# Performance work log

Hardware: AMD Instinct MI355X
Metric: run time of the kernel (lower is better)

Reference implementation:

```python
import jax, jax.numpy as jnp
import numpy as np

N_NODES = 50000
N_EDGES = 150000
HID = 512

def _gelu(x):
    return jax.nn.gelu(x, approximate=False)  # torch nn.GELU default is exact erf

def setup_inputs() -> dict:
    key = jax.random.key(0)
    ks = jax.random.split(key, 12)
    s = 0.02
    return {
        "node_features": jax.random.normal(ks[0], (N_NODES, HID), jnp.float32),
        "river_features": jax.random.normal(ks[1], (N_NODES, 3), jnp.float32),
        "river_edges": jax.random.randint(ks[2], (N_EDGES, 2), 0, N_NODES, jnp.int64),
        "W1": jax.random.normal(ks[3], (HID + 3, HID), jnp.float32) * s,
        "b1": jnp.zeros((HID,), jnp.float32),
        "W2": jax.random.normal(ks[4], (HID, HID), jnp.float32) * s,
        "b2": jnp.zeros((HID,), jnp.float32),
        "Wm1": jax.random.normal(ks[5], (2 * HID, HID), jnp.float32) * s,
        "bm1": jnp.zeros((HID,), jnp.float32),
        "Wm2": jax.random.normal(ks[6], (HID, HID), jnp.float32) * s,
        "bm2": jnp.zeros((HID,), jnp.float32),
    }

def _message_pass(features, edges, Wm1, bm1, Wm2, bm2):
    src = features[edges[:, 0]]   # [E, H] gather
    tgt = features[edges[:, 1]]   # [E, H] gather
    h = _gelu(jnp.concatenate([src, tgt], axis=-1) @ Wm1 + bm1)
    messages = h @ Wm2 + bm2      # [E, H]
    # the original per-edge python loop `new_features[tgt] += messages[i]` is a scatter-add
    return features + jax.ops.segment_sum(messages, edges[:, 1], num_segments=features.shape[0])

def reference(node_features, river_features, river_edges, W1, b1, W2, b2, Wm1, bm1, Wm2, bm2):
    x = jnp.concatenate([node_features, river_features], axis=-1)  # [N, H+3]
    feats = _gelu(x @ W1 + b1) @ W2 + b2                           # river_encoder
    for _ in range(3):
        feats = _message_pass(feats, river_edges, Wm1, bm1, Wm2, bm2)
    return feats
```

## Files before the change

### kernel.cpp

```cpp
#include <hip/hip_runtime.h>
#include <hip/hip_bf16.h>
#include <cstdint>

using u16 = unsigned short;
typedef short s16x8 __attribute__((ext_vector_type(8)));
typedef float f32x4 __attribute__((ext_vector_type(4)));

__device__ __forceinline__ float b2f(u16 b) {
    union { unsigned u; float f; } z; z.u = ((unsigned)b) << 16; return z.f;
}
__device__ __forceinline__ u16 f2b(float f) {
    union { float f; unsigned u; } z; z.f = f;
    return (u16)((z.u + 0x7fffu + ((z.u >> 16) & 1u)) >> 16);
}
__device__ __forceinline__ float gelu_f(float x) {
    return 0.5f * x * (1.0f + erff(x * 0.70710678118654752440f));
}
__device__ __forceinline__ void gl2lds16(const void* g, void* l) {
    __builtin_amdgcn_global_load_lds(
        (const __attribute__((address_space(1))) void*)g,
        (__attribute__((address_space(3))) void*)l, 16, 0, 0);
}

enum { F_BIAS = 1, F_GELU = 2, F_RANK3 = 4, F_RESIDH = 8,
       F_DEG = 16, F_OUTF = 32, F_OUTH = 64 };

template<int EPI>
__global__ __launch_bounds__(256, 4) void gemm_k(
    const u16* __restrict__ A, const u16* __restrict__ Bt,
    float* __restrict__ Cf, u16* __restrict__ Ch,
    const u16* __restrict__ srcH,
    const float* __restrict__ bias, const float* __restrict__ bias2,
    const int* __restrict__ deg, const float* __restrict__ river,
    const float* __restrict__ w1tail, int Mreal, int ldh, int gxShift)
{
    __shared__ __align__(16) u16 As[128 * 32];
    __shared__ __align__(16) u16 Bs[128 * 32];

    const int nwg  = gridDim.x;
    const int orig = blockIdx.x;
    const int xcd  = orig & 7;
    const int i    = orig >> 3;
    const int q    = nwg >> 3;
    const int r    = nwg & 7;
    const int swz  = (xcd < r) ? (xcd * (q + 1) + i) : (r * (q + 1) + (xcd - r) * q + i);
    const int rowblk = swz >> gxShift;
    const int colblk = swz & ((1 << gxShift) - 1);

    const int tid  = threadIdx.x;
    const int lane = tid & 63;
    const int wid  = tid >> 6;
    const int wr   = wid >> 1;
    const int wc   = wid & 1;
    const int fr   = lane & 15;
    const int fq   = lane >> 4;

    const long arow = (long)rowblk * 128 + (wid << 4) + (lane >> 2);
    const long brow = (long)colblk * 128 + (wid << 4) + (lane >> 2);
    const int  kofs = (lane & 3) << 3;
    u16* asw = As + (wid << 9);
    u16* bsw = Bs + (wid << 9);

    f32x4 acc[4][4];
#pragma unroll
    for (int m = 0; m < 4; m++)
#pragma unroll
        for (int n = 0; n < 4; n++) { f32x4 z = {0.f, 0.f, 0.f, 0.f}; acc[m][n] = z; }

    for (int kt = 0; kt < 512; kt += 32) {
        gl2lds16(A  + arow * 512 + kt + kofs,        asw);
        gl2lds16(A  + (arow + 64) * 512 + kt + kofs, asw + 2048);
        gl2lds16(Bt + brow * 512 + kt + kofs,        bsw);
        gl2lds16(Bt + (brow + 64) * 512 + kt + kofs, bsw + 2048);
        __syncthreads();

        s16x8 af[4], bf[4];
#pragma unroll
        for (int m = 0; m < 4; m++)
            af[m] = *(const s16x8*)(As + (((wr << 6) + (m << 4) + fr) << 5) + (fq << 3));
#pragma unroll
        for (int n = 0; n < 4; n++)
            bf[n] = *(const s16x8*)(Bs + (((wc << 6) + (n << 4) + fr) << 5) + (fq << 3));
#pragma unroll
        for (int m = 0; m < 4; m++)
#pragma unroll
            for (int n = 0; n < 4; n++)
                acc[m][n] = __builtin_amdgcn_mfma_f32_16x16x32_bf16(af[m], bf[n], acc[m][n], 0, 0, 0);
        __syncthreads();
    }

    const int colbase = (colblk << 7) + (wc << 6);
#pragma unroll
    for (int m = 0; m < 4; m++) {
        const int row0 = (rowblk << 7) + (wr << 6) + (m << 4) + (fq << 2);
#pragma unroll
        for (int rI = 0; rI < 4; rI++) {
            const int rr = row0 + rI;
            const bool real = rr < Mreal;
            float rv0 = 0.f, rv1 = 0.f, rv2 = 0.f;
            if constexpr (EPI & F_RANK3) {
                if (real) { rv0 = river[rr * 3]; rv1 = river[rr * 3 + 1]; rv2 = river[rr * 3 + 2]; }
            }
            float dg = 0.f;
            if constexpr (EPI & F_DEG) { if (real) dg = (float)deg[rr]; }
#pragma unroll
            for (int n = 0; n < 4; n++) {
                const int col = colbase + (n << 4) + fr;
                float v = acc[m][n][rI];
                if constexpr (EPI & F_BIAS)   v += bias[col];
                if constexpr (EPI & F_RANK3)  v += rv0 * w1tail[col] + rv1 * w1tail[512 + col] + rv2 * w1tail[1024 + col];
                if constexpr (EPI & F_GELU)   v = gelu_f(v);
                if constexpr (EPI & F_RESIDH) v += b2f(srcH[(long)rr * 512 + col]);
                if constexpr (EPI & F_DEG)    v += dg * bias2[col];
                if constexpr (EPI & F_OUTF)   { if (real) Cf[(long)rr * 512 + col] = v; }
                if constexpr (EPI & F_OUTH)   Ch[(long)rr * ldh + col] = f2b(v);
            }
        }
    }
}

__global__ __launch_bounds__(256) void deg_k(const int* __restrict__ ed, int* __restrict__ deg, int nE)
{
    const int e = blockIdx.x * 256 + threadIdx.x;
    if (e < nE) atomicAdd(&deg[ed[2 * e + 1]], 1);
}

__global__ __launch_bounds__(256) void scan1_k(
    const int* __restrict__ deg, int* __restrict__ rowptr,
    int* __restrict__ partials, int n)
{
    __shared__ int tmp[256];
    const int tid = threadIdx.x;
    const int gid = blockIdx.x * 256 + tid;
    const int v = (gid < n) ? deg[gid] : 0;
    tmp[tid] = v;
    __syncthreads();
#pragma unroll
    for (int ofs = 1; ofs < 256; ofs <<= 1) {
        int t = (tid >= ofs) ? tmp[tid - ofs] : 0;
        __syncthreads();
        tmp[tid] += t;
        __syncthreads();
    }
    if (gid < n) rowptr[gid] = tmp[tid] - v;
    if (tid == 255) partials[blockIdx.x] = tmp[255];
}

__global__ __launch_bounds__(256) void scan2_k(int* __restrict__ partials, int nb)
{
    __shared__ int tmp[256];
    const int tid = threadIdx.x;
    const int v = (tid < nb) ? partials[tid] : 0;
    tmp[tid] = v;
    __syncthreads();
#pragma unroll
    for (int ofs = 1; ofs < 256; ofs <<= 1) {
        int t = (tid >= ofs) ? tmp[tid - ofs] : 0;
        __syncthreads();
        tmp[tid] += t;
        __syncthreads();
    }
    if (tid < nb) partials[tid] = tmp[tid] - v;
}

__global__ __launch_bounds__(256) void scan3_k(
    int* __restrict__ rowptr, const int* __restrict__ partials, int n)
{
    const int gid = blockIdx.x * 256 + threadIdx.x;
    if (gid < n) rowptr[gid] += partials[blockIdx.x];
}

__global__ __launch_bounds__(256) void scat_k(
    const int* __restrict__ ed, const int* __restrict__ rowptr,
    int* __restrict__ cursor, int* __restrict__ csr, int nE)
{
    const int e = blockIdx.x * 256 + threadIdx.x;
    if (e >= nE) return;
    const int t = ed[2 * e + 1];
    const int p = atomicAdd(&cursor[t], 1);
    csr[rowptr[t] + p] = ed[2 * e];
}

__global__ __launch_bounds__(256) void gather_k(
    const int* __restrict__ rowptr, const int* __restrict__ degv,
    const int* __restrict__ csr, const u16* __restrict__ AB,
    const float* __restrict__ bm1, u16* __restrict__ Hg, int nNodes)
{
    const int t = (blockIdx.x << 2) + (threadIdx.x >> 6);
    if (t >= nNodes) return;
    const int lane = threadIdx.x & 63;
    const int c = lane << 3;
    float acc[8] = {0.f, 0.f, 0.f, 0.f, 0.f, 0.f, 0.f, 0.f};
    const int d = degv[t];
    if (d > 0) {
        s16x8 bv = *(const s16x8*)(AB + (long)t * 1024 + 512 + c);
        const float4* bmv = (const float4*)(bm1 + c);
        float4 q0 = bmv[0], q1 = bmv[1];
        float base[8] = { q0.x, q0.y, q0.z, q0.w, q1.x, q1.y, q1.z, q1.w };
#pragma unroll
        for (int j = 0; j < 8; j++) base[j] += b2f((u16)bv[j]);
        const int p0 = rowptr[t];
        for (int i = 0; i < d; i++) {
            const int s = csr[p0 + i];
            s16x8 av = *(const s16x8*)(AB + (long)s * 1024 + c);
#pragma unroll
            for (int j = 0; j < 8; j++) acc[j] += gelu_f(b2f((u16)av[j]) + base[j]);
        }
    }
    s16x8 o;
#pragma unroll
    for (int j = 0; j < 8; j++) o[j] = (short)f2b(acc[j]);
    *(s16x8*)(Hg + (long)t * 512 + c) = o;
}

__global__ __launch_bounds__(256) void cvt_pad_k(
    const float* __restrict__ src, u16* __restrict__ dst, long nSrc, long nTot)
{
    const long i = ((long)blockIdx.x * 256 + threadIdx.x) * 8;
    if (i >= nTot) return;
    s16x8 v;
    if (i + 8 <= nSrc) {
        const float4* s4 = (const float4*)(src + i);
        float4 a = s4[0], b = s4[1];
        v[0] = (short)f2b(a.x); v[1] = (short)f2b(a.y); v[2] = (short)f2b(a.z); v[3] = (short)f2b(a.w);
        v[4] = (short)f2b(b.x); v[5] = (short)f2b(b.y); v[6] = (short)f2b(b.z); v[7] = (short)f2b(b.w);
    } else {
#pragma unroll
        for (int j = 0; j < 8; j++) v[j] = (i + j < nSrc) ? (short)f2b(src[i + j]) : (short)0;
    }
    *(s16x8*)(dst + i) = v;
}

__global__ __launch_bounds__(256) void wtrans_k(
    const float* __restrict__ W, u16* __restrict__ Wt, int K, int N, int rowOff)
{
    const int idx = blockIdx.x * 256 + threadIdx.x;
    if (idx >= K * N) return;
    const int n = idx / K, k = idx % K;
    Wt[idx] = f2b(W[(long)(k + rowOff) * N + n]);
}

extern "C" void kernel_launch(void* const* d_in, const int* in_sizes, int n_in,
                              void* d_out, int out_size, void* d_ws, size_t ws_size,
                              hipStream_t stream)
{
    const float* nodef = (const float*)d_in[0];
    const float* river = (const float*)d_in[1];
    const int*   edges = (const int*)d_in[2];
    const float* W1  = (const float*)d_in[3];
    const float* b1  = (const float*)d_in[4];
    const float* W2  = (const float*)d_in[5];
    const float* b2  = (const float*)d_in[6];
    const float* Wm1 = (const float*)d_in[7];
    const float* bm1 = (const float*)d_in[8];
    const float* Wm2 = (const float*)d_in[9];
    const float* bm2 = (const float*)d_in[10];
    float* out = (float*)d_out;
    (void)n_in; (void)out_size;

    const int M = 50000, Mpad = 50048, H = 512;
    const int nE = in_sizes[2] / 2;
    const size_t nElem = (size_t)Mpad * H;
    const size_t nOut  = (size_t)M * H;

    char* ws = (char*)d_ws;
    size_t off = 0;
    auto alloc = [&](size_t bytes) { void* p = ws + off; off += (bytes + 255) & ~(size_t)255; return p; };
    u16* feats16 = (u16*)alloc(nElem * 2);
    u16* AB16    = (u16*)alloc(nElem * 4);
    u16* Hg16    = (u16*)alloc(nElem * 2);
    u16* W1t     = (u16*)alloc(512 * 512 * 2);
    u16* W2t     = (u16*)alloc(512 * 512 * 2);
    u16* Wm1ct   = (u16*)alloc(1024 * 512 * 2);
    u16* Wm2t    = (u16*)alloc(512 * 512 * 2);
    int* deg     = (int*)alloc((size_t)Mpad * 4);
    int* rowptr  = (int*)alloc((size_t)Mpad * 4);
    int* cursor  = (int*)alloc((size_t)Mpad * 4);
    int* csr     = (int*)alloc((size_t)nE * 4);
    int* partials= (int*)alloc(256 * 4);
    const size_t NEED = off;

    if (ws_size < NEED) return;

    const int scanBlocks = (Mpad + 255) / 256;
    const int MB = Mpad / 128;
    const dim3 g512(MB * 4, 1, 1);
    const dim3 g1024(MB * 8, 1, 1);
    const dim3 gblk(256, 1, 1);
    const int cvtBlocks = (int)(nElem / 8 / 256);

    hipMemsetAsync(deg, 0, (size_t)Mpad * 4, stream);
    hipMemsetAsync(cursor, 0, (size_t)Mpad * 4, stream);
    deg_k<<<dim3((nE + 255) / 256), gblk, 0, stream>>>(edges, deg, nE);
    scan1_k<<<dim3(scanBlocks), gblk, 0, stream>>>(deg, rowptr, partials, Mpad);
    scan2_k<<<dim3(1), gblk, 0, stream>>>(partials, scanBlocks);
    scan3_k<<<dim3(scanBlocks), gblk, 0, stream>>>(rowptr, partials, Mpad);
    scat_k<<<dim3((nE + 255) / 256), gblk, 0, stream>>>(edges, rowptr, cursor, csr, nE);

    wtrans_k<<<dim3(1024), gblk, 0, stream>>>(W1,  W1t,             512, 512, 0);
    wtrans_k<<<dim3(1024), gblk, 0, stream>>>(W2,  W2t,             512, 512, 0);
    wtrans_k<<<dim3(1024), gblk, 0, stream>>>(Wm1, Wm1ct,           512, 512, 0);
    wtrans_k<<<dim3(1024), gblk, 0, stream>>>(Wm1, Wm1ct + 512*512, 512, 512, 512);
    wtrans_k<<<dim3(1024), gblk, 0, stream>>>(Wm2, Wm2t,            512, 512, 0);

    cvt_pad_k<<<dim3(cvtBlocks), gblk, 0, stream>>>(nodef, AB16, (long)nOut, (long)nElem);

    gemm_k<F_BIAS | F_RANK3 | F_GELU | F_OUTH><<<g512, gblk, 0, stream>>>(
        AB16, W1t, nullptr, Hg16, nullptr, b1, nullptr, nullptr, river, W1 + 512 * 512, M, 512, 2);
    gemm_k<F_BIAS | F_OUTH><<<g512, gblk, 0, stream>>>(
        Hg16, W2t, nullptr, feats16, nullptr, b2, nullptr, nullptr, nullptr, nullptr, M, 512, 2);

    for (int r = 0; r < 3; r++) {
        gemm_k<F_OUTH><<<g1024, gblk, 0, stream>>>(
            feats16, Wm1ct, nullptr, AB16, nullptr, nullptr, nullptr, nullptr, nullptr, nullptr, M, 1024, 3);
        gather_k<<<dim3(Mpad / 4), gblk, 0, stream>>>(rowptr, deg, csr, AB16, bm1, Hg16, Mpad);
        if (r < 2)
            gemm_k<F_RESIDH | F_DEG | F_OUTH><<<g512, gblk, 0, stream>>>(
                Hg16, Wm2t, nullptr, feats16, feats16, nullptr, bm2, deg, nullptr, nullptr, M, 512, 2);
        else
            gemm_k<F_RESIDH | F_DEG | F_OUTF><<<g512, gblk, 0, stream>>>(
                Hg16, Wm2t, out, nullptr, feats16, nullptr, bm2, deg, nullptr, nullptr, M, 512, 2);
    }
}
```

Baseline: 671.2 us.

## Replace 128x128 GEMM with double-buffered 256x256 tile, 512-thread swizzled-LDS kernel

The bf16 MFMA GEMM moves from a 128x128 tile with K-step 32 and 256 threads to a 256x256 tile with K-step 64 and 512 threads (8 waves, each computing 128x64). LDS is double-buffered, so the next K slice is loaded while the current one is computed, and LDS chunks use an XOR swizzle to avoid bank conflicts. s_setprio is raised around the MFMA bursts. This aims to raise data reuse per byte loaded and hide global-load latency. The cost is about 128KB of LDS per block, which limits occupancy to one block per CU. It also means fewer, larger blocks, which risks wave-quantization tail imbalance, and padding M to 50176 adds some extra work.

```diff
diff --git a/kernel.cpp b/kernel.cpp
--- a/kernel.cpp
+++ b/kernel.cpp
@@ -26,7 +26,7 @@
        F_DEG = 16, F_OUTF = 32, F_OUTH = 64 };
 
 template<int EPI>
-__global__ __launch_bounds__(256, 4) void gemm_k(
+__global__ __launch_bounds__(512, 2) void gemm256_k(
     const u16* __restrict__ A, const u16* __restrict__ Bt,
     float* __restrict__ Cf, u16* __restrict__ Ch,
     const u16* __restrict__ srcH,
@@ -34,65 +34,92 @@
     const int* __restrict__ deg, const float* __restrict__ river,
     const float* __restrict__ w1tail, int Mreal, int ldh, int gxShift)
 {
-    __shared__ __align__(16) u16 As[128 * 32];
-    __shared__ __align__(16) u16 Bs[128 * 32];
+    __shared__ __align__(16) u16 smem[2][2][256 * 64];
 
     const int nwg  = gridDim.x;
     const int orig = blockIdx.x;
     const int xcd  = orig & 7;
-    const int i    = orig >> 3;
+    const int i8   = orig >> 3;
     const int q    = nwg >> 3;
-    const int r    = nwg & 7;
-    const int swz  = (xcd < r) ? (xcd * (q + 1) + i) : (r * (q + 1) + (xcd - r) * q + i);
+    const int rm   = nwg & 7;
+    const int swz  = (xcd < rm) ? (xcd * (q + 1) + i8)
+                                : (rm * (q + 1) + (xcd - rm) * q + i8);
     const int rowblk = swz >> gxShift;
     const int colblk = swz & ((1 << gxShift) - 1);
 
     const int tid  = threadIdx.x;
     const int lane = tid & 63;
-    const int wid  = tid >> 6;
-    const int wr   = wid >> 1;
-    const int wc   = wid & 1;
+    const int w    = tid >> 6;
+    const int wr   = w >> 2;
+    const int wc   = w & 3;
     const int fr   = lane & 15;
     const int fq   = lane >> 4;
 
-    const long arow = (long)rowblk * 128 + (wid << 4) + (lane >> 2);
-    const long brow = (long)colblk * 128 + (wid << 4) + (lane >> 2);
-    const int  kofs = (lane & 3) << 3;
-    u16* asw = As + (wid << 9);
-    u16* bsw = Bs + (wid << 9);
-
-    f32x4 acc[4][4];
-#pragma unroll
-    for (int m = 0; m < 4; m++)
+    const int  srow  = (w << 3) + (lane >> 3);
+    const long schnk = (long)(((lane & 7) ^ ((lane >> 3) & 7)) << 3);
+    const long abase = (long)rowblk * 256 + srow;
+    const long bbase = (long)colblk * 256 + srow;
+
+    auto STAGE = [&](int buf, int kt) {
+        u16* la = &smem[buf][0][0] + (w << 9);
+        u16* lb = &smem[buf][1][0] + (w << 9);
+        const long ko = (long)kt * 64 + schnk;
+#pragma unroll
+        for (int j = 0; j < 4; j++) {
+            gl2lds16(A  + (abase + j * 64) * 512 + ko, la + j * 4096);
+            gl2lds16(Bt + (bbase + j * 64) * 512 + ko, lb + j * 4096);
+        }
+    };
+
+    f32x4 acc[8][4];
+#pragma unroll
+    for (int m = 0; m < 8; m++)
 #pragma unroll
         for (int n = 0; n < 4; n++) { f32x4 z = {0.f, 0.f, 0.f, 0.f}; acc[m][n] = z; }
 
-    for (int kt = 0; kt < 512; kt += 32) {
-        gl2lds16(A  + arow * 512 + kt + kofs,        asw);
-        gl2lds16(A  + (arow + 64) * 512 + kt + kofs, asw + 2048);
-        gl2lds16(Bt + brow * 512 + kt + kofs,        bsw);
-        gl2lds16(Bt + (brow + 64) * 512 + kt + kofs, bsw + 2048);
-        __syncthreads();
-
-        s16x8 af[4], bf[4];
-#pragma unroll
-        for (int m = 0; m < 4; m++)
-            af[m] = *(const s16x8*)(As + (((wr << 6) + (m << 4) + fr) << 5) + (fq << 3));
-#pragma unroll
-        for (int n = 0; n < 4; n++)
-            bf[n] = *(const s16x8*)(Bs + (((wc << 6) + (n << 4) + fr) << 5) + (fq << 3));
-#pragma unroll
-        for (int m = 0; m < 4; m++)
+    STAGE(0, 0);
+    __syncthreads();
+
+    for (int kt = 0; kt < 8; kt++) {
+        const int cur = kt & 1;
+        if (kt < 7) STAGE(cur ^ 1, kt + 1);
+        const u16* Ab = &smem[cur][0][0];
+        const u16* Bb = &smem[cur][1][0];
+#pragma unroll
+        for (int ks = 0; ks < 2; ks++) {
+            const int sc = ((((ks << 2) + fq) ^ (fr & 7)) << 3);
+            s16x8 bf[4], af[4];
 #pragma unroll
             for (int n = 0; n < 4; n++)
-                acc[m][n] = __builtin_amdgcn_mfma_f32_16x16x32_bf16(af[m], bf[n], acc[m][n], 0, 0, 0);
-        __syncthreads();
-    }
-
-    const int colbase = (colblk << 7) + (wc << 6);
-#pragma unroll
-    for (int m = 0; m < 4; m++) {
-        const int row0 = (rowblk << 7) + (wr << 6) + (m << 4) + (fq << 2);
+                bf[n] = *(const s16x8*)(Bb + (((wc << 6) + (n << 4) + fr) << 6) + sc);
+#pragma unroll
+            for (int m = 0; m < 4; m++)
+                af[m] = *(const s16x8*)(Ab + (((wr << 7) + (m << 4) + fr) << 6) + sc);
+            __builtin_amdgcn_s_setprio(1);
+#pragma unroll
+            for (int m = 0; m < 4; m++)
+#pragma unroll
+                for (int n = 0; n < 4; n++)
+                    acc[m][n] = __builtin_amdgcn_mfma_f32_16x16x32_bf16(af[m], bf[n], acc[m][n], 0, 0, 0);
+            __builtin_amdgcn_s_setprio(0);
+#pragma unroll
+            for (int m = 0; m < 4; m++)
+                af[m] = *(const s16x8*)(Ab + (((wr << 7) + ((m + 4) << 4) + fr) << 6) + sc);
+            __builtin_amdgcn_s_setprio(1);
+#pragma unroll
+            for (int m = 0; m < 4; m++)
+#pragma unroll
+                for (int n = 0; n < 4; n++)
+                    acc[m + 4][n] = __builtin_amdgcn_mfma_f32_16x16x32_bf16(af[m], bf[n], acc[m + 4][n], 0, 0, 0);
+            __builtin_amdgcn_s_setprio(0);
+        }
+        __syncthreads();
+    }
+
+    const int colbase = (colblk << 8) + (wc << 6);
+#pragma unroll
+    for (int m = 0; m < 8; m++) {
+        const int row0 = (rowblk << 8) + (wr << 7) + (m << 4) + (fq << 2);
 #pragma unroll
         for (int rI = 0; rI < 4; rI++) {
             const int rr = row0 + rI;
@@ -258,7 +285,7 @@
     float* out = (float*)d_out;
     (void)n_in; (void)out_size;
 
-    const int M = 50000, Mpad = 50048, H = 512;
+    const int M = 50000, Mpad = 50176, H = 512;
     const int nE = in_sizes[2] / 2;
     const size_t nElem = (size_t)Mpad * H;
     const size_t nOut  = (size_t)M * H;
@@ -282,11 +309,11 @@
 
     if (ws_size < NEED) return;
 
-    const int scanBlocks = (Mpad + 255) / 256;
-    const int MB = Mpad / 128;
-    const dim3 g512(MB * 4, 1, 1);
-    const dim3 g1024(MB * 8, 1, 1);
+    const int scanBlocks = Mpad / 256;
+    const dim3 g512(scanBlocks * 2, 1, 1);
+    const dim3 g1024(scanBlocks * 4, 1, 1);
     const dim3 gblk(256, 1, 1);
+    const dim3 gblk512(512, 1, 1);
     const int cvtBlocks = (int)(nElem / 8 / 256);
 
     hipMemsetAsync(deg, 0, (size_t)Mpad * 4, stream);
@@ -305,20 +332,20 @@
 
     cvt_pad_k<<<dim3(cvtBlocks), gblk, 0, stream>>>(nodef, AB16, (long)nOut, (long)nElem);
 
-    gemm_k<F_BIAS | F_RANK3 | F_GELU | F_OUTH><<<g512, gblk, 0, stream>>>(
-        AB16, W1t, nullptr, Hg16, nullptr, b1, nullptr, nullptr, river, W1 + 512 * 512, M, 512, 2);
-    gemm_k<F_BIAS | F_OUTH><<<g512, gblk, 0, stream>>>(
-        Hg16, W2t, nullptr, feats16, nullptr, b2, nullptr, nullptr, nullptr, nullptr, M, 512, 2);
+    gemm256_k<F_BIAS | F_RANK3 | F_GELU | F_OUTH><<<g512, gblk512, 0, stream>>>(
+        AB16, W1t, nullptr, Hg16, nullptr, b1, nullptr, nullptr, river, W1 + 512 * 512, M, 512, 1);
+    gemm256_k<F_BIAS | F_OUTH><<<g512, gblk512, 0, stream>>>(
+        Hg16, W2t, nullptr, feats16, nullptr, b2, nullptr, nullptr, nullptr, nullptr, M, 512, 1);
 
     for (int r = 0; r < 3; r++) {
-        gemm_k<F_OUTH><<<g1024, gblk, 0, stream>>>(
-            feats16, Wm1ct, nullptr, AB16, nullptr, nullptr, nullptr, nullptr, nullptr, nullptr, M, 1024, 3);
+        gemm256_k<F_OUTH><<<g1024, gblk512, 0, stream>>>(
+            feats16, Wm1ct, nullptr, AB16, nullptr, nullptr, nullptr, nullptr, nullptr, nullptr, M, 1024, 2);
         gather_k<<<dim3(Mpad / 4), gblk, 0, stream>>>(rowptr, deg, csr, AB16, bm1, Hg16, Mpad);
         if (r < 2)
-            gemm_k<F_RESIDH | F_DEG | F_OUTH><<<g512, gblk, 0, stream>>>(
-                Hg16, Wm2t, nullptr, feats16, feats16, nullptr, bm2, deg, nullptr, nullptr, M, 512, 2);
+            gemm256_k<F_RESIDH | F_DEG | F_OUTH><<<g512, gblk512, 0, stream>>>(
+                Hg16, Wm2t, nullptr, feats16, feats16, nullptr, bm2, deg, nullptr, nullptr, M, 512, 1);
         else
-            gemm_k<F_RESIDH | F_DEG | F_OUTF><<<g512, gblk, 0, stream>>>(
-                Hg16, Wm2t, out, nullptr, feats16, nullptr, bm2, deg, nullptr, nullptr, M, 512, 2);
-    }
-}
+            gemm256_k<F_RESIDH | F_DEG | F_OUTF><<<g512, gblk512, 0, stream>>>(
+                Hg16, Wm2t, out, nullptr, feats16, nullptr, bm2, deg, nullptr, nullptr, M, 512, 1);
+    }
+}
```

Measured after the change: 728.4 us. +8.5%, slower.

## Fold Wm2 into Wm1 so message rounds chain through fused weights

Applied to the files above, without the earlier changes.

Precomputes Wfuse = Wm2·Wm1 plus a fused bias, so each later round's A/B projection comes straight from the aggregated hidden sum, skipping the separate Wm2 GEMM. The fused path updates AB in place through a residual term. It keeps a running sum of the gathered hidden states so one final Wm2 GEMM (bias scaled by 3·deg) produces the output. This trades three 512-wide GEMMs plus two 1024-wide GEMMs for two fused 1024-wide GEMMs plus one final GEMM. It adds extra bf16 rounding through the fused weights and the accumulated sum, and the in-place residual on AB may be a hazard.

```diff
diff --git a/kernel.cpp b/kernel.cpp
--- a/kernel.cpp
+++ b/kernel.cpp
@@ -32,7 +32,8 @@
     const u16* __restrict__ srcH,
     const float* __restrict__ bias, const float* __restrict__ bias2,
     const int* __restrict__ deg, const float* __restrict__ river,
-    const float* __restrict__ w1tail, int Mreal, int ldh, int gxShift)
+    const float* __restrict__ w1tail, int Mreal, int ldh, int gxShift,
+    float degScale)
 {
     __shared__ __align__(16) u16 As[128 * 32];
     __shared__ __align__(16) u16 Bs[128 * 32];
@@ -40,10 +41,11 @@
     const int nwg  = gridDim.x;
     const int orig = blockIdx.x;
     const int xcd  = orig & 7;
-    const int i    = orig >> 3;
+    const int i8   = orig >> 3;
     const int q    = nwg >> 3;
-    const int r    = nwg & 7;
-    const int swz  = (xcd < r) ? (xcd * (q + 1) + i) : (r * (q + 1) + (xcd - r) * q + i);
+    const int rm   = nwg & 7;
+    const int swz  = (xcd < rm) ? (xcd * (q + 1) + i8)
+                                : (rm * (q + 1) + (xcd - rm) * q + i8);
     const int rowblk = swz >> gxShift;
     const int colblk = swz & ((1 << gxShift) - 1);
 
@@ -102,7 +104,7 @@
                 if (real) { rv0 = river[rr * 3]; rv1 = river[rr * 3 + 1]; rv2 = river[rr * 3 + 2]; }
             }
             float dg = 0.f;
-            if constexpr (EPI & F_DEG) { if (real) dg = (float)deg[rr]; }
+            if constexpr (EPI & F_DEG) { if (real) dg = (float)deg[rr] * degScale; }
 #pragma unroll
             for (int n = 0; n < 4; n++) {
                 const int col = colbase + (n << 4) + fr;
@@ -110,7 +112,7 @@
                 if constexpr (EPI & F_BIAS)   v += bias[col];
                 if constexpr (EPI & F_RANK3)  v += rv0 * w1tail[col] + rv1 * w1tail[512 + col] + rv2 * w1tail[1024 + col];
                 if constexpr (EPI & F_GELU)   v = gelu_f(v);
-                if constexpr (EPI & F_RESIDH) v += b2f(srcH[(long)rr * 512 + col]);
+                if constexpr (EPI & F_RESIDH) v += b2f(srcH[(long)rr * ldh + col]);
                 if constexpr (EPI & F_DEG)    v += dg * bias2[col];
                 if constexpr (EPI & F_OUTF)   { if (real) Cf[(long)rr * 512 + col] = v; }
                 if constexpr (EPI & F_OUTH)   Ch[(long)rr * ldh + col] = f2b(v);
@@ -184,7 +186,8 @@
 __global__ __launch_bounds__(256) void gather_k(
     const int* __restrict__ rowptr, const int* __restrict__ degv,
     const int* __restrict__ csr, const u16* __restrict__ AB,
-    const float* __restrict__ bm1, u16* __restrict__ Hg, int nNodes)
+    const float* __restrict__ bm1, u16* __restrict__ Hg,
+    u16* __restrict__ Hsum, int accum, int nNodes)
 {
     const int t = (blockIdx.x << 2) + (threadIdx.x >> 6);
     if (t >= nNodes) return;
@@ -207,10 +210,24 @@
             for (int j = 0; j < 8; j++) acc[j] += gelu_f(b2f((u16)av[j]) + base[j]);
         }
     }
-    s16x8 o;
-#pragma unroll
-    for (int j = 0; j < 8; j++) o[j] = (short)f2b(acc[j]);
-    *(s16x8*)(Hg + (long)t * 512 + c) = o;
+    if (Hg) {
+        s16x8 o;
+#pragma unroll
+        for (int j = 0; j < 8; j++) o[j] = (short)f2b(acc[j]);
+        *(s16x8*)(Hg + (long)t * 512 + c) = o;
+    }
+    if (Hsum) {
+        s16x8 o;
+        if (accum) {
+            s16x8 old = *(const s16x8*)(Hsum + (long)t * 512 + c);
+#pragma unroll
+            for (int j = 0; j < 8; j++) o[j] = (short)f2b(b2f((u16)old[j]) + acc[j]);
+        } else {
+#pragma unroll
+            for (int j = 0; j < 8; j++) o[j] = (short)f2b(acc[j]);
+        }
+        *(s16x8*)(Hsum + (long)t * 512 + c) = o;
+    }
 }
 
 __global__ __launch_bounds__(256) void cvt_pad_k(
@@ -238,6 +255,22 @@
     if (idx >= K * N) return;
     const int n = idx / K, k = idx % K;
     Wt[idx] = f2b(W[(long)(k + rowOff) * N + n]);
+}
+
+__global__ __launch_bounds__(256) void bfuse_k(
+    const float* __restrict__ bm2, const u16* __restrict__ Wm1ct,
+    float* __restrict__ bfuse)
+{
+    const int j = blockIdx.x * 256 + threadIdx.x;
+    if (j >= 1024) return;
+    float s = 0.f;
+    const u16* row = Wm1ct + (long)j * 512;
+    for (int k = 0; k < 512; k += 8) {
+        s16x8 w = *(const s16x8*)(row + k);
+#pragma unroll
+        for (int u = 0; u < 8; u++) s += bm2[k + u] * b2f((u16)w[u]);
+    }
+    bfuse[j] = s;
 }
 
 extern "C" void kernel_launch(void* const* d_in, const int* in_sizes, int n_in,
@@ -278,14 +311,21 @@
     int* cursor  = (int*)alloc((size_t)Mpad * 4);
     int* csr     = (int*)alloc((size_t)nE * 4);
     int* partials= (int*)alloc(256 * 4);
-    const size_t NEED = off;
-
-    if (ws_size < NEED) return;
+    const size_t NEED_BASE = off;
+    u16* Hsum16  = (u16*)alloc(nElem * 2);
+    u16* Wfuset  = (u16*)alloc(1024 * 512 * 2);
+    u16* Wm2nt   = (u16*)alloc(512 * 512 * 2);
+    float* bfuse = (float*)alloc(1024 * 4);
+    const size_t NEED_FUSED = off;
+
+    if (ws_size < NEED_BASE) return;
+    const bool fused = ws_size >= NEED_FUSED;
 
     const int scanBlocks = (Mpad + 255) / 256;
     const int MB = Mpad / 128;
     const dim3 g512(MB * 4, 1, 1);
     const dim3 g1024(MB * 8, 1, 1);
+    const dim3 gtiny(32, 1, 1);
     const dim3 gblk(256, 1, 1);
     const int cvtBlocks = (int)(nElem / 8 / 256);
 
@@ -306,19 +346,38 @@
     cvt_pad_k<<<dim3(cvtBlocks), gblk, 0, stream>>>(nodef, AB16, (long)nOut, (long)nElem);
 
     gemm_k<F_BIAS | F_RANK3 | F_GELU | F_OUTH><<<g512, gblk, 0, stream>>>(
-        AB16, W1t, nullptr, Hg16, nullptr, b1, nullptr, nullptr, river, W1 + 512 * 512, M, 512, 2);
+        AB16, W1t, nullptr, Hg16, nullptr, b1, nullptr, nullptr, river, W1 + 512 * 512, M, 512, 2, 1.f);
     gemm_k<F_BIAS | F_OUTH><<<g512, gblk, 0, stream>>>(
-        Hg16, W2t, nullptr, feats16, nullptr, b2, nullptr, nullptr, nullptr, nullptr, M, 512, 2);
-
-    for (int r = 0; r < 3; r++) {
+        Hg16, W2t, nullptr, feats16, nullptr, b2, nullptr, nullptr, nullptr, nullptr, M, 512, 2, 1.f);
+
+    if (fused) {
+        cvt_pad_k<<<dim3(128), gblk, 0, stream>>>(Wm2, Wm2nt, 512 * 512, 512 * 512);
+        gemm_k<F_OUTH><<<gtiny, gblk, 0, stream>>>(
+            Wm1ct, Wm2nt, nullptr, Wfuset, nullptr, nullptr, nullptr, nullptr, nullptr, nullptr, 1024, 512, 2, 1.f);
+        bfuse_k<<<dim3(4), gblk, 0, stream>>>(bm2, Wm1ct, bfuse);
+
         gemm_k<F_OUTH><<<g1024, gblk, 0, stream>>>(
-            feats16, Wm1ct, nullptr, AB16, nullptr, nullptr, nullptr, nullptr, nullptr, nullptr, M, 1024, 3);
-        gather_k<<<dim3(Mpad / 4), gblk, 0, stream>>>(rowptr, deg, csr, AB16, bm1, Hg16, Mpad);
-        if (r < 2)
-            gemm_k<F_RESIDH | F_DEG | F_OUTH><<<g512, gblk, 0, stream>>>(
-                Hg16, Wm2t, nullptr, feats16, feats16, nullptr, bm2, deg, nullptr, nullptr, M, 512, 2);
-        else
-            gemm_k<F_RESIDH | F_DEG | F_OUTF><<<g512, gblk, 0, stream>>>(
-                Hg16, Wm2t, out, nullptr, feats16, nullptr, bm2, deg, nullptr, nullptr, M, 512, 2);
-    }
-}
+            feats16, Wm1ct, nullptr, AB16, nullptr, nullptr, nullptr, nullptr, nullptr, nullptr, M, 1024, 3, 1.f);
+        gather_k<<<dim3(Mpad / 4), gblk, 0, stream>>>(rowptr, deg, csr, AB16, bm1, nullptr, Hsum16, 0, Mpad);
+        gemm_k<F_RESIDH | F_DEG | F_OUTH><<<g1024, gblk, 0, stream>>>(
+            Hsum16, Wfuset, nullptr, AB16, AB16, nullptr, bfuse, deg, nullptr, nullptr, M, 1024, 3, 1.f);
+        gather_k<<<dim3(Mpad / 4), gblk, 0, stream>>>(rowptr, deg, csr, AB16, bm1, Hg16, Hsum16, 1, Mpad);
+        gemm_k<F_RESIDH | F_DEG | F_OUTH><<<g1024, gblk, 0, stream>>>(
+            Hg16, Wfuset, nullptr, AB16, AB16, nullptr, bfuse, deg, nullptr, nullptr, M, 1024, 3, 1.f);
+        gather_k<<<dim3(Mpad / 4), gblk, 0, stream>>>(rowptr, deg, csr, AB16, bm1, nullptr, Hsum16, 1, Mpad);
+        gemm_k<F_RESIDH | F_DEG | F_OUTF><<<g512, gblk, 0, stream>>>(
+            Hsum16, Wm2t, out, nullptr, feats16, nullptr, bm2, deg, nullptr, nullptr, M, 512, 2, 3.f);
+    } else {
+        for (int r = 0; r < 3; r++) {
+            gemm_k<F_OUTH><<<g1024, gblk, 0, stream>>>(
+                feats16, Wm1ct, nullptr, AB16, nullptr, nullptr, nullptr, nullptr, nullptr, nullptr, M, 1024, 3, 1.f);
+            gather_k<<<dim3(Mpad / 4), gblk, 0, stream>>>(rowptr, deg, csr, AB16, bm1, Hg16, nullptr, 0, Mpad);
+            if (r < 2)
+                gemm_k<F_RESIDH | F_DEG | F_OUTH><<<g512, gblk, 0, stream>>>(
+                    Hg16, Wm2t, nullptr, feats16, feats16, nullptr, bm2, deg, nullptr, nullptr, M, 512, 2, 1.f);
+            else
+                gemm_k<F_RESIDH | F_DEG | F_OUTF><<<g512, gblk, 0, stream>>>(
+                    Hg16, Wm2t, out, nullptr, feats16, nullptr, bm2, deg, nullptr, nullptr, M, 512, 2, 1.f);
+        }
+    }
+}
```

Result: slower. 690.1 us (+2.8%).
